# Kernel tuning notes

Measured on AMD Instinct MI355X. Metric: run time of the kernel, lower is better.

The kernel has to match this reference:

```python
import jax, jax.numpy as jnp
import numpy as np

N_LAYERS, B, H, D = 24, 16, 32, 64
E = H * D            # 2048
TS_H = 32            # token_shift_hidden_dim
N_BRANCH = 5         # key, receptance, decay, value, bonus
GN_EPS = 1e-3        # keras GroupNormalization default epsilon


def setup_inputs() -> dict:
    key = jax.random.key(0)
    ks = jax.random.split(key, 20)
    s = 0.02
    return {
        "inputs": jax.random.normal(ks[0], (B, E), jnp.float32),
        "state": jax.random.normal(ks[1], (N_LAYERS, 1, B, E), jnp.float32),
        "state_matrix": jax.random.normal(ks[2], (N_LAYERS, B, H, D, D), jnp.float32),
        # stacked branch params, order: key, receptance, decay, value, bonus
        "mus": jax.random.normal(ks[3], (N_BRANCH, E), jnp.float32) * s,
        "lambdas": jax.random.normal(ks[4], (N_BRANCH, E), jnp.float32) * s,
        "Aw": jax.random.normal(ks[5], (N_BRANCH, E, TS_H), jnp.float32) * s,
        "Ab": jnp.zeros((N_BRANCH, TS_H), jnp.float32),
        "Bw": jax.random.normal(ks[6], (N_BRANCH, TS_H, E), jnp.float32) * s,
        "Bb": jnp.zeros((N_BRANCH, E), jnp.float32),
        "MW": jax.random.normal(ks[7], (N_BRANCH, H, D, D), jnp.float32) * s,
        "Mb": jnp.zeros((N_BRANCH, H, D), jnp.float32),
        "gate_mu": jax.random.normal(ks[8], (E,), jnp.float32) * s,
        "gate_W": jax.random.normal(ks[9], (E, E), jnp.float32) * s,
        "gate_b": jnp.zeros((E,), jnp.float32),
        "gn_gamma": jnp.ones((E,), jnp.float32),
        "gn_beta": jnp.zeros((E,), jnp.float32),
        "out_W": jax.random.normal(ks[10], (E, E), jnp.float32) * s,
        "out_b": jnp.zeros((E,), jnp.float32),
        "layer_id": 12,
    }


def reference(inputs, state, state_matrix, mus, lambdas, Aw, Ab, Bw, Bb, MW, Mb,
              gate_mu, gate_W, gate_b, gn_gamma, gn_beta, out_W, out_b, layer_id):
    x = inputs                       # [B, E]
    last_x = state[layer_id, 0]      # [B, E]
    diff = x - last_x

    # ddlerp token shift for all 5 branches at once:
    # lora(x + diff*mu) = lambda + tanh(. @ A) @ B ; out = x + lora * diff
    lora_in = x[None] + diff[None] * mus[:, None]                      # [5, B, E]
    hdn = jnp.tanh(jnp.einsum('sbe,seh->sbh', lora_in, Aw) + Ab[:, None])
    lora = jnp.einsum('sbh,she->sbe', hdn, Bw) + Bb[:, None] + lambdas[:, None]
    ts = (lora * diff[None] + x[None]).reshape(N_BRANCH, B, H, D)      # [5, B, H, D]

    # per-head dense for each branch
    proj = jnp.einsum('sbhd,shde->sbhe', ts, MW) + Mb[:, None]         # [5, B, H, D]
    k, r, w_raw, v, u = proj[0], proj[1], proj[2], proj[3], proj[4]

    g = (x * gate_mu + last_x * (1.0 - gate_mu)) @ gate_W + gate_b     # [B, E]

    kv = k[..., :, None] * v[..., None, :]                             # [B, H, D, D]
    w = jnp.exp(-jnp.exp(w_raw))[..., None]                            # [B, H, D, 1]
    S = state_matrix[layer_id]                                         # [B, H, D, D]
    wkv = kv * u[..., None] + S
    new_S = w * S + kv
    rwkv = jnp.einsum('bhij,bhj->bhi', wkv, r)                         # [B, H, D]

    # group norm: num_heads groups over channel axis
    mean = rwkv.mean(-1, keepdims=True)
    var = rwkv.var(-1, keepdims=True)
    normed = ((rwkv - mean) / jnp.sqrt(var + GN_EPS)).reshape(B, E)
    normed = normed * gn_gamma + gn_beta

    time_mixed = (normed * jax.nn.silu(g)) @ out_W + out_b             # [B, E]

    new_state = state.at[layer_id, 0].set(inputs)
    new_state_matrix = state_matrix.at[layer_id].set(new_S)
    return time_mixed, new_state, new_state_matrix
```

## Files before the change

### kernel.cpp

```cpp
#include <hip/hip_runtime.h>
#include <math.h>

#define NL 24
#define BB 16
#define HH 32
#define DD 64
#define EE 2048
#define TSH 32
#define NB 5
#define BE (BB*EE)
#define STATE_N (NL*BB*EE)
#define GN_EPS 1e-3f

#define NCH 11776
#define C1 3300
#define C2 3200
#define C3 3200
#define C4 2076

typedef float nt4 __attribute__((ext_vector_type(4)));

__device__ __forceinline__ void sm_chunk(int c, int lid, const nt4* __restrict__ sm4,
                                         nt4* __restrict__ out4, int tid) {
    int l = c >> 9, rr = c & 511;
    int ls = l + (l >= lid);
    const nt4* src = sm4 + (long)(ls * 512 + rr) * 1024;
    nt4*       dst = out4 + (long)(ls * 512 + rr) * 1024;
    #pragma unroll
    for (int p = 0; p < 4; ++p) {
        nt4 v = __builtin_nontemporal_load(&src[p * 256 + tid]);
        __builtin_nontemporal_store(v, &dst[p * 256 + tid]);
    }
}

__global__ __launch_bounds__(256) void k1_hdn(
    const float* __restrict__ inputs, const float* __restrict__ state,
    const float* __restrict__ mus, const float* __restrict__ Aw,
    const float* __restrict__ Ab, float* __restrict__ hdn,
    const nt4* __restrict__ state4, const float4* __restrict__ inputs4,
    nt4* __restrict__ out_state4, float* __restrict__ out_tm,
    float* __restrict__ g, const float* __restrict__ out_b,
    const float* __restrict__ gate_b, const float* __restrict__ gate_mu,
    float* __restrict__ gx,
    const nt4* __restrict__ sm4, nt4* __restrict__ out_sm4,
    const int* __restrict__ lid_p)
{
    int blk = blockIdx.x, tid = threadIdx.x;
    int lid = *lid_p;
    if (blk >= 1232) {
        sm_chunk(blk - 1232, lid, sm4, out_sm4, tid);
        return;
    }
    if (blk >= 848) {
        int idx = (blk - 848) * 256 + tid;
        if (idx < BE) out_tm[idx] = out_b[idx & (EE - 1)];
        else if (idx < 2 * BE) g[idx - BE] = gate_b[(idx - BE) & (EE - 1)];
        else {
            int r = idx - 2 * BE;
            float xv = inputs[r];
            float lxv = state[lid * BE + r];
            float gm = gate_mu[r & (EE - 1)];
            gx[r] = xv * gm + lxv * (1.f - gm);
        }
        return;
    }
    if (blk >= 80) {
        int i = (blk - 80) * 256 + tid;
        int lo = lid * (BE / 4);
        if (i >= lo && i < lo + BE / 4) {
            float4 v = inputs4[i - lo];
            nt4 w = { v.x, v.y, v.z, v.w };
            __builtin_nontemporal_store(w, &out_state4[i]);
        } else {
            nt4 v = __builtin_nontemporal_load(&state4[i]);
            __builtin_nontemporal_store(v, &out_state4[i]);
        }
        return;
    }
    int s = blk / BB, b = blk % BB;
    __shared__ float li[EE];
    const float* x  = inputs + b * EE;
    const float* lx = state + lid * BE + b * EE;
    const float* mu = mus + s * EE;
    for (int e = tid; e < EE; e += 256) {
        float xv = x[e];
        li[e] = xv + (xv - lx[e]) * mu[e];
    }
    __syncthreads();
    int h = tid & 31, part = tid >> 5;
    const float* A = Aw + s * EE * TSH;
    float acc = 0.f;
    int e0 = part * 256;
    #pragma unroll 8
    for (int e = e0; e < e0 + 256; ++e) acc += li[e] * A[e * TSH + h];
    __shared__ float red[32][9];
    red[h][part] = acc;
    __syncthreads();
    if (tid < 32) {
        float sum = Ab[s * TSH + tid];
        #pragma unroll
        for (int p = 0; p < 8; ++p) sum += red[tid][p];
        hdn[(s * BB + b) * TSH + tid] = tanhf(sum);
    }
}

template <bool SILU>
__device__ __forceinline__ void mm_block(
    int t, const float* __restrict__ Arows, const float* __restrict__ Grows,
    const float* __restrict__ W, float* __restrict__ out, int tid)
{
    int et = t & 7, kc = t >> 3;
    int e = et * 256 + tid;
    int k0 = kc * 64;
    __shared__ float As[BB][64];
    for (int i = tid; i < BB * 64; i += 256) {
        int b = i >> 6, kk = i & 63;
        float av = Arows[b * EE + k0 + kk];
        if constexpr (SILU) {
            float gv = Grows[b * EE + k0 + kk];
            av *= gv / (1.f + expf(-gv));
        }
        As[b][kk] = av;
    }
    __syncthreads();
    float acc[BB];
    #pragma unroll
    for (int b = 0; b < BB; ++b) acc[b] = 0.f;
    #pragma unroll 8
    for (int kk = 0; kk < 64; ++kk) {
        float wv = W[(k0 + kk) * EE + e];
        #pragma unroll
        for (int b = 0; b < BB; ++b) acc[b] += As[b][kk] * wv;
    }
    #pragma unroll
    for (int b = 0; b < BB; ++b) atomicAdd(&out[b * EE + e], acc[b]);
}

__global__ __launch_bounds__(256) void k2_tsproj(
    const float* __restrict__ inputs, const float* __restrict__ state,
    const float* __restrict__ lambdas, const float* __restrict__ Bw,
    const float* __restrict__ Bb, const float* __restrict__ hdn,
    const float* __restrict__ MW, const float* __restrict__ Mb,
    float* __restrict__ proj,
    const float* __restrict__ gx, const float* __restrict__ gate_W,
    float* __restrict__ g,
    const nt4* __restrict__ sm4, nt4* __restrict__ out_sm4,
    const int* __restrict__ lid_p)
{
    int blk = blockIdx.x, tid = threadIdx.x;
    if (blk >= 896) {
        int lid = *lid_p;
        sm_chunk(C1 + blk - 896, lid, sm4, out_sm4, tid);
        return;
    }
    if (blk >= 640) {
        mm_block<false>(blk - 640, gx, nullptr, gate_W, g, tid);
        return;
    }
    int lid = *lid_p;
    int s = blk / (BB * 8);
    int r = blk % (BB * 8);
    int b = r / 8, hg = r % 8;
    int e = hg * 256 + tid;
    __shared__ float hl[TSH];
    __shared__ float tsl[256];
    if (tid < TSH) hl[tid] = hdn[(s * BB + b) * TSH + tid];
    __syncthreads();
    {
        int ge = b * EE + e;
        const float* Bp = Bw + s * TSH * EE + e;
        float acc = Bb[s * EE + e] + lambdas[s * EE + e];
        #pragma unroll
        for (int h = 0; h < TSH; ++h) acc += hl[h] * Bp[h * EE];
        float xv = inputs[ge];
        float lxv = state[lid * BE + ge];
        tsl[tid] = acc * (xv - lxv) + xv;
    }
    __syncthreads();
    int q = tid >> 6, e2 = tid & 63;
    int h = hg * 4 + q;
    const float* M = MW + (s * HH + h) * DD * DD;
    const float* t = tsl + q * DD;
    float acc = Mb[(s * HH + h) * DD + e2];
    #pragma unroll 8
    for (int d = 0; d < DD; ++d) acc += t[d] * M[d * DD + e2];
    proj[((s * BB + b) * HH + h) * DD + e2] = acc;
}

__global__ __launch_bounds__(256) void k3_rwkv(
    const float4* __restrict__ sm4, float4* __restrict__ out_sm4,
    const float* __restrict__ proj,
    const float* __restrict__ gn_gamma, const float* __restrict__ gn_beta,
    float* __restrict__ a_out, const int* __restrict__ lid_p)
{
    int blk = blockIdx.x, tid = threadIdx.x;
    int lid = *lid_p;
    if (blk >= 512) {
        sm_chunk(C1 + C2 + blk - 512, lid,
                 (const nt4*)sm4, (nt4*)out_sm4, tid);
        return;
    }
    int b = blk / HH, h = blk % HH;
    long base4 = (long)(lid * BB * HH + blk) * (DD * DD / 4);
    int j = tid & 63, q = tid >> 6;
    const float* P = proj + (b * HH + h) * DD + j;
    float kv   = P[0 * BE];
    float rv   = P[1 * BE];
    float wraw = P[2 * BE];
    float vv   = P[3 * BE];
    float uv   = P[4 * BE];
    float wv = expf(-expf(wraw));
    float vr = vv * rv;
    #pragma unroll
    for (int o = 32; o; o >>= 1) vr += __shfl_xor(vr, o);
    __shared__ float rw[DD];
    const float* S = (const float*)(sm4 + base4);
    float* NS = (float*)(out_sm4 + base4);
    for (int ii = 0; ii < 16; ii += 4) {
        int i0 = q * 16 + ii;
        float sv[4], kk[4], ww[4], uu[4], pp[4];
        #pragma unroll
        for (int t = 0; t < 4; ++t) {
            sv[t] = S[(i0 + t) * DD + j];
            kk[t] = __shfl(kv, i0 + t);
            ww[t] = __shfl(wv, i0 + t);
            uu[t] = __shfl(uv, i0 + t);
        }
        #pragma unroll
        for (int t = 0; t < 4; ++t) {
            NS[(i0 + t) * DD + j] = ww[t] * sv[t] + kk[t] * vv;
            pp[t] = sv[t] * rv;
        }
        #pragma unroll
        for (int o = 32; o; o >>= 1) {
            #pragma unroll
            for (int t = 0; t < 4; ++t) pp[t] += __shfl_xor(pp[t], o);
        }
        if (j == 0) {
            #pragma unroll
            for (int t = 0; t < 4; ++t) rw[i0 + t] = kk[t] * uu[t] * vr + pp[t];
        }
    }
    __syncthreads();
    if (tid < DD) {
        float xv = rw[tid];
        float m = xv;
        #pragma unroll
        for (int o = 32; o; o >>= 1) m += __shfl_xor(m, o);
        m *= (1.f / 64.f);
        float d = xv - m;
        float var = d * d;
        #pragma unroll
        for (int o = 32; o; o >>= 1) var += __shfl_xor(var, o);
        var *= (1.f / 64.f);
        float normed = d * rsqrtf(var + GN_EPS);
        int e = h * DD + tid;
        a_out[b * EE + e] = normed * gn_gamma[e] + gn_beta[e];
    }
}

__global__ __launch_bounds__(256) void k4_out(
    const float* __restrict__ a, const float* __restrict__ g,
    const float* __restrict__ out_W, float* __restrict__ out_tm,
    const nt4* __restrict__ sm4, nt4* __restrict__ out_sm4,
    const int* __restrict__ lid_p)
{
    int blk = blockIdx.x, tid = threadIdx.x;
    if (blk < 256) { mm_block<true>(blk, a, g, out_W, out_tm, tid); return; }
    int lid = *lid_p;
    sm_chunk(C1 + C2 + C3 + blk - 256, lid, sm4, out_sm4, tid);
}

extern "C" void kernel_launch(void* const* d_in, const int* in_sizes, int n_in,
                              void* d_out, int out_size, void* d_ws, size_t ws_size,
                              hipStream_t stream) {
    const float* inputs   = (const float*)d_in[0];
    const float* state    = (const float*)d_in[1];
    const float* sm       = (const float*)d_in[2];
    const float* mus      = (const float*)d_in[3];
    const float* lambdas  = (const float*)d_in[4];
    const float* Aw       = (const float*)d_in[5];
    const float* Ab       = (const float*)d_in[6];
    const float* Bw       = (const float*)d_in[7];
    const float* Bb       = (const float*)d_in[8];
    const float* MW       = (const float*)d_in[9];
    const float* Mb       = (const float*)d_in[10];
    const float* gate_mu  = (const float*)d_in[11];
    const float* gate_W   = (const float*)d_in[12];
    const float* gate_b   = (const float*)d_in[13];
    const float* gn_gamma = (const float*)d_in[14];
    const float* gn_beta  = (const float*)d_in[15];
    const float* out_W    = (const float*)d_in[16];
    const float* out_b    = (const float*)d_in[17];
    const int*   lid      = (const int*)d_in[18];

    float* out_tm    = (float*)d_out;
    float* out_state = out_tm + BE;
    float* out_sm    = out_state + STATE_N;

    float* ws   = (float*)d_ws;
    float* proj = ws;
    float* hdn  = proj + NB * BE;
    float* gx   = hdn + NB * BB * TSH;
    float* g    = gx + BE;
    float* a    = g + BE;

    k1_hdn<<<1232 + C1, 256, 0, stream>>>(inputs, state, mus, Aw, Ab, hdn,
        (const nt4*)state, (const float4*)inputs, (nt4*)out_state,
        out_tm, g, out_b, gate_b, gate_mu, gx,
        (const nt4*)sm, (nt4*)out_sm, lid);
    k2_tsproj<<<896 + C2, 256, 0, stream>>>(inputs, state, lambdas, Bw, Bb, hdn,
        MW, Mb, proj, gx, gate_W, g,
        (const nt4*)sm, (nt4*)out_sm, lid);
    k3_rwkv<<<512 + C3, 256, 0, stream>>>((const float4*)sm, (float4*)out_sm,
        proj, gn_gamma, gn_beta, a, lid);
    k4_out<<<256 + C4, 256, 0, stream>>>(a, g, out_W, out_tm,
        (const nt4*)sm, (nt4*)out_sm, lid);
}
```

Before: 429.1 us.

## Merge four kernels into three by fusing hdn into branch projection

The tanh(lora@A) step is fused into the branch projection kernel. Each of the 640 blocks now recomputes its own hdn vector, which removes the hdn round-trip through global memory and one kernel launch boundary. The gate projection moves into the rwkv kernel and computes its mixed input inline, so the gx buffer is gone. The state_matrix copy chunks are spread across three launches instead of four. The cost is redundant work: each (s,b) pair recomputes the 2048x32 A projection 8 times, adding Aw reads.

```diff
diff --git a/kernel.cpp b/kernel.cpp
--- a/kernel.cpp
+++ b/kernel.cpp
@@ -13,10 +13,9 @@
 #define GN_EPS 1e-3f
 
 #define NCH 11776
-#define C1 3300
-#define C2 3200
-#define C3 3200
-#define C4 2076
+#define CA 4600
+#define CB 4600
+#define CC 2576
 
 typedef float nt4 __attribute__((ext_vector_type(4)));
 
@@ -33,39 +32,34 @@
     }
 }
 
-__global__ __launch_bounds__(256) void k1_hdn(
+__global__ __launch_bounds__(256) void kA_branch(
     const float* __restrict__ inputs, const float* __restrict__ state,
     const float* __restrict__ mus, const float* __restrict__ Aw,
-    const float* __restrict__ Ab, float* __restrict__ hdn,
+    const float* __restrict__ Ab, const float* __restrict__ lambdas,
+    const float* __restrict__ Bw, const float* __restrict__ Bb,
+    const float* __restrict__ MW, const float* __restrict__ Mb,
+    float* __restrict__ proj,
     const nt4* __restrict__ state4, const float4* __restrict__ inputs4,
     nt4* __restrict__ out_state4, float* __restrict__ out_tm,
     float* __restrict__ g, const float* __restrict__ out_b,
-    const float* __restrict__ gate_b, const float* __restrict__ gate_mu,
-    float* __restrict__ gx,
+    const float* __restrict__ gate_b,
     const nt4* __restrict__ sm4, nt4* __restrict__ out_sm4,
     const int* __restrict__ lid_p)
 {
     int blk = blockIdx.x, tid = threadIdx.x;
     int lid = *lid_p;
-    if (blk >= 1232) {
-        sm_chunk(blk - 1232, lid, sm4, out_sm4, tid);
-        return;
-    }
-    if (blk >= 848) {
-        int idx = (blk - 848) * 256 + tid;
+    if (blk >= 1664) {
+        sm_chunk(blk - 1664, lid, sm4, out_sm4, tid);
+        return;
+    }
+    if (blk >= 1408) {
+        int idx = (blk - 1408) * 256 + tid;
         if (idx < BE) out_tm[idx] = out_b[idx & (EE - 1)];
-        else if (idx < 2 * BE) g[idx - BE] = gate_b[(idx - BE) & (EE - 1)];
-        else {
-            int r = idx - 2 * BE;
-            float xv = inputs[r];
-            float lxv = state[lid * BE + r];
-            float gm = gate_mu[r & (EE - 1)];
-            gx[r] = xv * gm + lxv * (1.f - gm);
-        }
-        return;
-    }
-    if (blk >= 80) {
-        int i = (blk - 80) * 256 + tid;
+        else g[idx - BE] = gate_b[(idx - BE) & (EE - 1)];
+        return;
+    }
+    if (blk >= 640) {
+        int i = (blk - 640) * 256 + tid;
         int lo = lid * (BE / 4);
         if (i >= lo && i < lo + BE / 4) {
             float4 v = inputs4[i - lo];
@@ -77,8 +71,13 @@
         }
         return;
     }
-    int s = blk / BB, b = blk % BB;
+    int s = blk / (BB * 8);
+    int r = blk % (BB * 8);
+    int b = r / 8, hg = r % 8;
     __shared__ float li[EE];
+    __shared__ float red[TSH][9];
+    __shared__ float hdnl[TSH];
+    __shared__ float tsl[256];
     const float* x  = inputs + b * EE;
     const float* lx = state + lid * BE + b * EE;
     const float* mu = mus + s * EE;
@@ -87,93 +86,31 @@
         li[e] = xv + (xv - lx[e]) * mu[e];
     }
     __syncthreads();
-    int h = tid & 31, part = tid >> 5;
-    const float* A = Aw + s * EE * TSH;
-    float acc = 0.f;
-    int e0 = part * 256;
-    #pragma unroll 8
-    for (int e = e0; e < e0 + 256; ++e) acc += li[e] * A[e * TSH + h];
-    __shared__ float red[32][9];
-    red[h][part] = acc;
-    __syncthreads();
-    if (tid < 32) {
+    {
+        int h = tid & 31, part = tid >> 5;
+        const float* A = Aw + s * EE * TSH;
+        float acc = 0.f;
+        int e0 = part * 256;
+        #pragma unroll 8
+        for (int e = e0; e < e0 + 256; ++e) acc += li[e] * A[e * TSH + h];
+        red[h][part] = acc;
+    }
+    __syncthreads();
+    if (tid < TSH) {
         float sum = Ab[s * TSH + tid];
         #pragma unroll
         for (int p = 0; p < 8; ++p) sum += red[tid][p];
-        hdn[(s * BB + b) * TSH + tid] = tanhf(sum);
-    }
-}
-
-template <bool SILU>
-__device__ __forceinline__ void mm_block(
-    int t, const float* __restrict__ Arows, const float* __restrict__ Grows,
-    const float* __restrict__ W, float* __restrict__ out, int tid)
-{
-    int et = t & 7, kc = t >> 3;
-    int e = et * 256 + tid;
-    int k0 = kc * 64;
-    __shared__ float As[BB][64];
-    for (int i = tid; i < BB * 64; i += 256) {
-        int b = i >> 6, kk = i & 63;
-        float av = Arows[b * EE + k0 + kk];
-        if constexpr (SILU) {
-            float gv = Grows[b * EE + k0 + kk];
-            av *= gv / (1.f + expf(-gv));
-        }
-        As[b][kk] = av;
-    }
-    __syncthreads();
-    float acc[BB];
-    #pragma unroll
-    for (int b = 0; b < BB; ++b) acc[b] = 0.f;
-    #pragma unroll 8
-    for (int kk = 0; kk < 64; ++kk) {
-        float wv = W[(k0 + kk) * EE + e];
-        #pragma unroll
-        for (int b = 0; b < BB; ++b) acc[b] += As[b][kk] * wv;
-    }
-    #pragma unroll
-    for (int b = 0; b < BB; ++b) atomicAdd(&out[b * EE + e], acc[b]);
-}
-
-__global__ __launch_bounds__(256) void k2_tsproj(
-    const float* __restrict__ inputs, const float* __restrict__ state,
-    const float* __restrict__ lambdas, const float* __restrict__ Bw,
-    const float* __restrict__ Bb, const float* __restrict__ hdn,
-    const float* __restrict__ MW, const float* __restrict__ Mb,
-    float* __restrict__ proj,
-    const float* __restrict__ gx, const float* __restrict__ gate_W,
-    float* __restrict__ g,
-    const nt4* __restrict__ sm4, nt4* __restrict__ out_sm4,
-    const int* __restrict__ lid_p)
-{
-    int blk = blockIdx.x, tid = threadIdx.x;
-    if (blk >= 896) {
-        int lid = *lid_p;
-        sm_chunk(C1 + blk - 896, lid, sm4, out_sm4, tid);
-        return;
-    }
-    if (blk >= 640) {
-        mm_block<false>(blk - 640, gx, nullptr, gate_W, g, tid);
-        return;
-    }
-    int lid = *lid_p;
-    int s = blk / (BB * 8);
-    int r = blk % (BB * 8);
-    int b = r / 8, hg = r % 8;
-    int e = hg * 256 + tid;
-    __shared__ float hl[TSH];
-    __shared__ float tsl[256];
-    if (tid < TSH) hl[tid] = hdn[(s * BB + b) * TSH + tid];
+        hdnl[tid] = tanhf(sum);
+    }
     __syncthreads();
     {
-        int ge = b * EE + e;
+        int e = hg * 256 + tid;
         const float* Bp = Bw + s * TSH * EE + e;
         float acc = Bb[s * EE + e] + lambdas[s * EE + e];
         #pragma unroll
-        for (int h = 0; h < TSH; ++h) acc += hl[h] * Bp[h * EE];
-        float xv = inputs[ge];
-        float lxv = state[lid * BE + ge];
+        for (int h = 0; h < TSH; ++h) acc += hdnl[h] * Bp[h * EE];
+        float xv = x[e];
+        float lxv = lx[e];
         tsl[tid] = acc * (xv - lxv) + xv;
     }
     __syncthreads();
@@ -187,17 +124,60 @@
     proj[((s * BB + b) * HH + h) * DD + e2] = acc;
 }
 
-__global__ __launch_bounds__(256) void k3_rwkv(
+template <int MODE>
+__device__ __forceinline__ void mm_block(
+    int t, const float* __restrict__ A1, const float* __restrict__ A2,
+    const float* __restrict__ gmu,
+    const float* __restrict__ W, float* __restrict__ out, int tid)
+{
+    int et = t & 7, kc = t >> 3;
+    int e = et * 256 + tid;
+    int k0 = kc * 64;
+    __shared__ float As[BB][64];
+    for (int i = tid; i < BB * 64; i += 256) {
+        int b = i >> 6, kk = i & 63;
+        int idx = b * EE + k0 + kk;
+        float av;
+        if constexpr (MODE == 1) {
+            float gv = A2[idx];
+            av = A1[idx] * (gv / (1.f + expf(-gv)));
+        } else {
+            float gm = gmu[k0 + kk];
+            av = A1[idx] * gm + A2[idx] * (1.f - gm);
+        }
+        As[b][kk] = av;
+    }
+    __syncthreads();
+    float acc[BB];
+    #pragma unroll
+    for (int b = 0; b < BB; ++b) acc[b] = 0.f;
+    #pragma unroll 8
+    for (int kk = 0; kk < 64; ++kk) {
+        float wv = W[(k0 + kk) * EE + e];
+        #pragma unroll
+        for (int b = 0; b < BB; ++b) acc[b] += As[b][kk] * wv;
+    }
+    #pragma unroll
+    for (int b = 0; b < BB; ++b) atomicAdd(&out[b * EE + e], acc[b]);
+}
+
+__global__ __launch_bounds__(256) void kB_rwkv(
     const float4* __restrict__ sm4, float4* __restrict__ out_sm4,
     const float* __restrict__ proj,
     const float* __restrict__ gn_gamma, const float* __restrict__ gn_beta,
-    float* __restrict__ a_out, const int* __restrict__ lid_p)
+    float* __restrict__ a_out,
+    const float* __restrict__ inputs, const float* __restrict__ state,
+    const float* __restrict__ gate_mu, const float* __restrict__ gate_W,
+    float* __restrict__ g, const int* __restrict__ lid_p)
 {
     int blk = blockIdx.x, tid = threadIdx.x;
     int lid = *lid_p;
+    if (blk >= 768) {
+        sm_chunk(CA + blk - 768, lid, (const nt4*)sm4, (nt4*)out_sm4, tid);
+        return;
+    }
     if (blk >= 512) {
-        sm_chunk(C1 + C2 + blk - 512, lid,
-                 (const nt4*)sm4, (nt4*)out_sm4, tid);
+        mm_block<2>(blk - 512, inputs, state + lid * BE, gate_mu, gate_W, g, tid);
         return;
     }
     int b = blk / HH, h = blk % HH;
@@ -259,16 +239,16 @@
     }
 }
 
-__global__ __launch_bounds__(256) void k4_out(
+__global__ __launch_bounds__(256) void kC_out(
     const float* __restrict__ a, const float* __restrict__ g,
     const float* __restrict__ out_W, float* __restrict__ out_tm,
     const nt4* __restrict__ sm4, nt4* __restrict__ out_sm4,
     const int* __restrict__ lid_p)
 {
     int blk = blockIdx.x, tid = threadIdx.x;
-    if (blk < 256) { mm_block<true>(blk, a, g, out_W, out_tm, tid); return; }
+    if (blk < 256) { mm_block<1>(blk, a, g, nullptr, out_W, out_tm, tid); return; }
     int lid = *lid_p;
-    sm_chunk(C1 + C2 + C3 + blk - 256, lid, sm4, out_sm4, tid);
+    sm_chunk(CA + CB + blk - 256, lid, sm4, out_sm4, tid);
 }
 
 extern "C" void kernel_launch(void* const* d_in, const int* in_sizes, int n_in,
@@ -300,20 +280,16 @@
 
     float* ws   = (float*)d_ws;
     float* proj = ws;
-    float* hdn  = proj + NB * BE;
-    float* gx   = hdn + NB * BB * TSH;
-    float* g    = gx + BE;
+    float* g    = proj + NB * BE;
     float* a    = g + BE;
 
-    k1_hdn<<<1232 + C1, 256, 0, stream>>>(inputs, state, mus, Aw, Ab, hdn,
+    kA_branch<<<1664 + CA, 256, 0, stream>>>(inputs, state, mus, Aw, Ab,
+        lambdas, Bw, Bb, MW, Mb, proj,
         (const nt4*)state, (const float4*)inputs, (nt4*)out_state,
-        out_tm, g, out_b, gate_b, gate_mu, gx,
+        out_tm, g, out_b, gate_b,
         (const nt4*)sm, (nt4*)out_sm, lid);
-    k2_tsproj<<<896 + C2, 256, 0, stream>>>(inputs, state, lambdas, Bw, Bb, hdn,
-        MW, Mb, proj, gx, gate_W, g,
+    kB_rwkv<<<768 + CB, 256, 0, stream>>>((const float4*)sm, (float4*)out_sm,
+        proj, gn_gamma, gn_beta, a, inputs, state, gate_mu, gate_W, g, lid);
+    kC_out<<<256 + CC, 256, 0, stream>>>(a, g, out_W, out_tm,
         (const nt4*)sm, (nt4*)out_sm, lid);
-    k3_rwkv<<<512 + C3, 256, 0, stream>>>((const float4*)sm, (float4*)out_sm,
-        proj, gn_gamma, gn_beta, a, lid);
-    k4_out<<<256 + C4, 256, 0, stream>>>(a, g, out_W, out_tm,
-        (const nt4*)sm, (nt4*)out_sm, lid);
-}
+}
```

Result: faster. 417.8 us (-2.6%).
